# Kernel optimization log

Measured on AMD Instinct MI355X. Metric: run time of the kernel, lower is better.

## Reference

```python
import jax, jax.numpy as jnp
import numpy as np

N = 10000   # num_nodes (= input feature dim, identity-style features)
E = 320000  # edges (avg degree 32)
P = 200000  # candidate node pairs
H1, H2 = 32, 16


def gcn_conv(x, W, b, edge_index, num_nodes):
    # PyG GCNConv: add self-loops, symmetric D^-1/2 (A+I) D^-1/2 normalization,
    # linear transform, scatter-add aggregation, then bias.
    loop = jnp.arange(num_nodes)
    src = jnp.concatenate([edge_index[0], loop])
    dst = jnp.concatenate([edge_index[1], loop])
    deg = jax.ops.segment_sum(jnp.ones_like(src, dtype=x.dtype), dst,
                              num_segments=num_nodes)  # includes self-loop, so deg >= 1
    dinv = jax.lax.rsqrt(deg)
    norm = dinv[src] * dinv[dst]                       # [E+N]
    h = x @ W                                          # [N, out]
    out = jax.ops.segment_sum(h[src] * norm[:, None], dst, num_segments=num_nodes)
    return out + b


def setup_inputs() -> dict:
    key = jax.random.key(0)
    ks = jax.random.split(key, 9)
    x = jax.random.normal(ks[0], (N, N), dtype=jnp.float32)
    edge_index = jax.random.randint(ks[1], (2, E), 0, N)
    pair_index = jax.random.randint(ks[2], (P, 2), 0, N)
    W1 = jax.random.normal(ks[3], (N, H1), dtype=jnp.float32) * 0.01
    b1 = jnp.zeros((H1,), jnp.float32)
    W2 = jax.random.normal(ks[4], (H1, H2), dtype=jnp.float32) * 0.1
    b2 = jnp.zeros((H2,), jnp.float32)
    Wfc = jax.random.normal(ks[5], (2 * H2, 1), dtype=jnp.float32) * 0.1
    bfc = jnp.zeros((1,), jnp.float32)
    return {"x": x, "edge_index": edge_index, "pair_index": pair_index,
            "W1": W1, "b1": b1, "W2": W2, "b2": b2, "Wfc": Wfc, "bfc": bfc}


def reference(x, edge_index, pair_index, W1, b1, W2, b2, Wfc, bfc):
    h = jax.nn.relu(gcn_conv(x, W1, b1, edge_index, N))   # [N, 32]
    h = gcn_conv(h, W2, b2, edge_index, N)                # [N, 16]
    pair = jnp.concatenate([h[pair_index[:, 0]], h[pair_index[:, 1]]], axis=1)  # [P, 32]
    return jax.nn.sigmoid(pair @ Wfc + bfc)               # [P, 1]
```

## Files before the change

kernel.cpp:

```cpp
#include <hip/hip_runtime.h>
#include <math.h>

#define NN 10000
#define EE 320000
#define PP 200000

typedef __attribute__((ext_vector_type(8))) short bf8v;
typedef __attribute__((ext_vector_type(4))) float f4v;

#define GLOAD_LDS16(gsrc, ldst)                                                        \
    __builtin_amdgcn_global_load_lds((const __attribute__((address_space(1))) void*)(gsrc), \
                                     (__attribute__((address_space(3))) void*)(ldst), 16, 0, 0)

__device__ __forceinline__ ushort f2bf(float f) {
    uint u = __float_as_uint(f);
    return (ushort)((u + 0x7fffu + ((u >> 16) & 1u)) >> 16);
}

__global__ void k_deg_count(const int* __restrict__ dst, int* __restrict__ degi) {
    int e = blockIdx.x * blockDim.x + threadIdx.x;
    if (e < EE) atomicAdd(&degi[dst[e]], 1);
}

__global__ void k_dinv(const int* __restrict__ degi, float* __restrict__ dinv) {
    int n = blockIdx.x * blockDim.x + threadIdx.x;
    if (n < NN) dinv[n] = rsqrtf((float)(degi[n] + 1));
}

__global__ __launch_bounds__(256) void k_gemm1(const float* __restrict__ x,
                                               const float* __restrict__ W1,
                                               const float* __restrict__ zp,
                                               float* __restrict__ h1_pre) {
    __shared__ __align__(16) float  xs[2][128][32];
    __shared__ __align__(16) ushort wt[2][32][32];
    const int tid = threadIdx.x;
    const int lane = tid & 63;
    const int w = tid >> 6;
    const int lr = lane >> 3;
    const int s = lane & 7;
    const int row0 = blockIdx.x * 128;
    const int k_begin = blockIdx.y * 640;
    const int k_end = min(NN, k_begin + 640);
    const int ntiles = (k_end - k_begin + 31) >> 5;
    const long NN2 = (long)NN * NN;

    const int wc = tid & 31;
    const int wkq = tid >> 5;
    const int wt_off = wc * 32 + ((((wkq >> 1) ^ (wc & 3))) << 3) + ((wkq & 1) << 2);

    const int fl = lane & 15;
    const int khi = lane >> 4;

    f4v acc[2][2];
#pragma unroll
    for (int a = 0; a < 2; ++a)
#pragma unroll
        for (int b = 0; b < 2; ++b) acc[a][b] = (f4v){0.f, 0.f, 0.f, 0.f};

    auto stage_x = [&](int buf, int k0) {
#pragma unroll
        for (int j = 0; j < 4; ++j) {
            int r_local = w * 32 + j * 8 + lr;
            int c4 = s ^ (r_local & 7);
            long flat = (long)(row0 + r_local) * NN + k0 + c4 * 4;
            const float* src = (flat + 4 <= NN2) ? (x + flat) : zp;
            GLOAD_LDS16(src, &xs[buf][w * 32 + j * 8][0]);
        }
    };
    auto wload = [&](int k0, float* wr) {
#pragma unroll
        for (int i = 0; i < 4; ++i) {
            int gk = k0 + wkq * 4 + i;
            wr[i] = (gk < k_end) ? W1[(long)gk * 32 + wc] : 0.f;
        }
    };
    auto wstore = [&](int buf, const float* wr) {
        union { uint2 d; ushort u[4]; } p;
        p.u[0] = f2bf(wr[0]); p.u[1] = f2bf(wr[1]);
        p.u[2] = f2bf(wr[2]); p.u[3] = f2bf(wr[3]);
        *(uint2*)((ushort*)&wt[buf][0][0] + wt_off) = p.d;
    };
    auto compute = [&](int buf) {
        bf8v bfr[2];
        const int nb = fl & 3;
#pragma unroll
        for (int ct = 0; ct < 2; ++ct)
            bfr[ct] = *(const bf8v*)&wt[buf][ct * 16 + fl][(khi ^ nb) << 3];
#pragma unroll
        for (int rt = 0; rt < 2; ++rt) {
            const int row = w * 32 + rt * 16 + fl;
            const float4* xr = (const float4*)&xs[buf][row][0];
            float4 f0 = xr[(khi * 2) ^ (row & 7)];
            float4 f1 = xr[(khi * 2 + 1) ^ (row & 7)];
            union { bf8v v; ushort u[8]; } a;
            a.u[0] = f2bf(f0.x); a.u[1] = f2bf(f0.y); a.u[2] = f2bf(f0.z); a.u[3] = f2bf(f0.w);
            a.u[4] = f2bf(f1.x); a.u[5] = f2bf(f1.y); a.u[6] = f2bf(f1.z); a.u[7] = f2bf(f1.w);
#pragma unroll
            for (int ct = 0; ct < 2; ++ct)
                acc[rt][ct] = __builtin_amdgcn_mfma_f32_16x16x32_bf16(a.v, bfr[ct], acc[rt][ct], 0, 0, 0);
        }
    };

    float wr0[4], wr1[4];
    wload(k_begin, wr0);
    stage_x(0, k_begin);
    wstore(0, wr0);
    __syncthreads();

    int buf = 0;
    for (int t = 0; t < ntiles; ++t) {
        const int k0n = k_begin + (t + 1) * 32;
        if (t + 1 < ntiles) { wload(k0n, wr1); stage_x(buf ^ 1, k0n); }
        compute(buf);
        if (t + 1 < ntiles) wstore(buf ^ 1, wr1);
        __syncthreads();
        buf ^= 1;
    }

#pragma unroll
    for (int rt = 0; rt < 2; ++rt) {
        const int gbase = row0 + w * 32 + rt * 16 + khi * 4;
#pragma unroll
        for (int ct = 0; ct < 2; ++ct) {
            const int col = ct * 16 + fl;
#pragma unroll
            for (int r = 0; r < 4; ++r) {
                const int g = gbase + r;
                if (g < NN) atomicAdd(&h1_pre[g * 32 + col], acc[rt][ct][r]);
            }
        }
    }
}

__global__ void k_selfinit1(const float* __restrict__ h1_pre, const float* __restrict__ dinv,
                            float* __restrict__ out1) {
    int t = blockIdx.x * blockDim.x + threadIdx.x;
    if (t < NN * 32) {
        int n = t >> 5;
        float di = dinv[n];
        out1[t] = di * di * h1_pre[t];
    }
}

__global__ void k_scatter1(const int* __restrict__ src, const int* __restrict__ dst,
                           const float* __restrict__ dinv, const float* __restrict__ h1_pre,
                           float* __restrict__ out1) {
    int t = blockIdx.x * blockDim.x + threadIdx.x;
    if (t >= EE * 32) return;
    int e = t >> 5, c = t & 31;
    int s = src[e], d = dst[e];
    float nrm = dinv[s] * dinv[d];
    atomicAdd(&out1[d * 32 + c], h1_pre[s * 32 + c] * nrm);
}

__global__ void k_bias_relu1(float* __restrict__ out1, const float* __restrict__ b1) {
    int t = blockIdx.x * blockDim.x + threadIdx.x;
    if (t < NN * 32) out1[t] = fmaxf(out1[t] + b1[t & 31], 0.f);
}

__global__ __launch_bounds__(256) void k_gemm2(const float* __restrict__ out1,
                                               const float* __restrict__ W2,
                                               float* __restrict__ h2_pre) {
    __shared__ float w2s[512];
    int tid = threadIdx.x;
    w2s[tid] = W2[tid & 511];
    if (tid < 256) w2s[256 + tid] = W2[256 + tid];
    __syncthreads();
    int c = tid & 15, yloc = tid >> 4;
    int n = blockIdx.x * 16 + yloc;
    if (n < NN) {
        float a = 0.f;
#pragma unroll
        for (int k = 0; k < 32; ++k) a += out1[n * 32 + k] * w2s[k * 16 + c];
        h2_pre[n * 16 + c] = a;
    }
}

__global__ void k_selfinit2(const float* __restrict__ h2_pre, const float* __restrict__ dinv,
                            float* __restrict__ out2) {
    int t = blockIdx.x * blockDim.x + threadIdx.x;
    if (t < NN * 16) {
        int n = t >> 4;
        float di = dinv[n];
        out2[t] = di * di * h2_pre[t];
    }
}

__global__ void k_scatter2(const int* __restrict__ src, const int* __restrict__ dst,
                           const float* __restrict__ dinv, const float* __restrict__ h2_pre,
                           float* __restrict__ out2) {
    int t = blockIdx.x * blockDim.x + threadIdx.x;
    if (t >= EE * 16) return;
    int e = t >> 4, c = t & 15;
    int s = src[e], d = dst[e];
    float nrm = dinv[s] * dinv[d];
    atomicAdd(&out2[d * 16 + c], h2_pre[s * 16 + c] * nrm);
}

__global__ void k_final2(const float* __restrict__ out2, const float* __restrict__ b2,
                         const float* __restrict__ Wfc, float* __restrict__ s_arr,
                         float* __restrict__ t_arr) {
    int n = blockIdx.x * blockDim.x + threadIdx.x;
    if (n >= NN) return;
    float s = 0.f, t = 0.f;
#pragma unroll
    for (int c = 0; c < 16; ++c) {
        float v = out2[n * 16 + c] + b2[c];
        s += v * Wfc[c];
        t += v * Wfc[16 + c];
    }
    s_arr[n] = s;
    t_arr[n] = t;
}

__global__ void k_pairs(const int* __restrict__ pair, const float* __restrict__ s_arr,
                        const float* __restrict__ t_arr, const float* __restrict__ bfc,
                        float* __restrict__ out) {
    int p = blockIdx.x * blockDim.x + threadIdx.x;
    if (p >= PP) return;
    const int2 ab = ((const int2*)pair)[p];
    float z = s_arr[ab.x] + t_arr[ab.y] + bfc[0];
    out[p] = 1.f / (1.f + expf(-z));
}

extern "C" void kernel_launch(void* const* d_in, const int* in_sizes, int n_in,
                              void* d_out, int out_size, void* d_ws, size_t ws_size,
                              hipStream_t stream) {
    const float* x    = (const float*)d_in[0];
    const int*   edge = (const int*)d_in[1];
    const int*   pair = (const int*)d_in[2];
    const float* W1   = (const float*)d_in[3];
    const float* b1   = (const float*)d_in[4];
    const float* W2   = (const float*)d_in[5];
    const float* b2   = (const float*)d_in[6];
    const float* Wfc  = (const float*)d_in[7];
    const float* bfc  = (const float*)d_in[8];
    float* out = (float*)d_out;
    float* ws  = (float*)d_ws;

    const int* src = edge;
    const int* dst = edge + EE;

    int*   degi   = (int*)ws;
    float* dinv   = ws + NN;
    float* h1_pre = ws + 2 * NN;
    float* out1   = ws + 34 * NN;
    float* h2_pre = ws + 66 * NN;
    float* out2   = ws + 82 * NN;
    float* s_arr  = ws + 98 * NN;
    float* t_arr  = ws + 99 * NN;
    float* zp     = ws + 100 * NN;

    hipMemsetAsync(degi, 0, NN * sizeof(int), stream);
    hipMemsetAsync(h1_pre, 0, NN * 32 * sizeof(float), stream);
    hipMemsetAsync(zp, 0, 1024, stream);

    k_deg_count<<<(EE + 255) / 256, 256, 0, stream>>>(dst, degi);
    k_dinv<<<(NN + 255) / 256, 256, 0, stream>>>(degi, dinv);

    k_gemm1<<<dim3(79, 16), 256, 0, stream>>>(x, W1, zp, h1_pre);

    k_selfinit1<<<(NN * 32 + 255) / 256, 256, 0, stream>>>(h1_pre, dinv, out1);
    k_scatter1<<<(EE * 32 + 255) / 256, 256, 0, stream>>>(src, dst, dinv, h1_pre, out1);
    k_bias_relu1<<<(NN * 32 + 255) / 256, 256, 0, stream>>>(out1, b1);

    k_gemm2<<<(NN + 15) / 16, 256, 0, stream>>>(out1, W2, h2_pre);

    k_selfinit2<<<(NN * 16 + 255) / 256, 256, 0, stream>>>(h2_pre, dinv, out2);
    k_scatter2<<<(EE * 16 + 255) / 256, 256, 0, stream>>>(src, dst, dinv, h2_pre, out2);

    k_final2<<<(NN + 255) / 256, 256, 0, stream>>>(out2, b2, Wfc, s_arr, t_arr);
    k_pairs<<<(PP + 255) / 256, 256, 0, stream>>>(pair, s_arr, t_arr, bfc, out);
}
```

Baseline: 204.4 us.

## Pre-transpose W1 to bf16 and triple-buffer per-wave x staging without block syncs

Adds a prep kernel that transposes W1 to column-major bf16, so the GEMM loads B fragments straight from global memory into registers instead of converting and staging them through LDS. The x tiles are now staged per wave in a three-deep ring buffer, with a vmcnt wait replacing __syncthreads, which lets each wave prefetch two tiles ahead on its own. The aim is to remove block-wide barriers and the LDS round trip for weights, so the first GEMM streams the large x matrix closer to memory bandwidth. It costs an extra kernel launch, and the hand-written waitcnt depends on counting exactly how many loads are in flight.

```diff
diff --git a/kernel.cpp b/kernel.cpp
--- a/kernel.cpp
+++ b/kernel.cpp
@@ -4,6 +4,7 @@
 #define NN 10000
 #define EE 320000
 #define PP 200000
+#define WKP 10240
 
 typedef __attribute__((ext_vector_type(8))) short bf8v;
 typedef __attribute__((ext_vector_type(4))) float f4v;
@@ -27,99 +28,88 @@
     if (n < NN) dinv[n] = rsqrtf((float)(degi[n] + 1));
 }
 
+__global__ void k_wprep(const float* __restrict__ W1, ushort* __restrict__ w1t) {
+    int t = blockIdx.x * blockDim.x + threadIdx.x;
+    if (t >= 32 * WKP) return;
+    int c = t / WKP, k = t - c * WKP;
+    float v = (k < NN) ? W1[(long)k * 32 + c] : 0.f;
+    w1t[t] = f2bf(v);
+}
+
 __global__ __launch_bounds__(256) void k_gemm1(const float* __restrict__ x,
-                                               const float* __restrict__ W1,
+                                               const ushort* __restrict__ w1t,
                                                const float* __restrict__ zp,
                                                float* __restrict__ h1_pre) {
-    __shared__ __align__(16) float  xs[2][128][32];
-    __shared__ __align__(16) ushort wt[2][32][32];
+    __shared__ __align__(16) float xs[4][3][32][32];
     const int tid = threadIdx.x;
     const int lane = tid & 63;
     const int w = tid >> 6;
     const int lr = lane >> 3;
     const int s = lane & 7;
-    const int row0 = blockIdx.x * 128;
+    const int fl = lane & 15;
+    const int khi = lane >> 4;
+    const int row0 = blockIdx.x * 128 + w * 32;
     const int k_begin = blockIdx.y * 640;
     const int k_end = min(NN, k_begin + 640);
-    const int ntiles = (k_end - k_begin + 31) >> 5;
+    const int nt = (k_end - k_begin + 31) >> 5;
     const long NN2 = (long)NN * NN;
 
-    const int wc = tid & 31;
-    const int wkq = tid >> 5;
-    const int wt_off = wc * 32 + ((((wkq >> 1) ^ (wc & 3))) << 3) + ((wkq & 1) << 2);
-
-    const int fl = lane & 15;
-    const int khi = lane >> 4;
-
     f4v acc[2][2];
 #pragma unroll
     for (int a = 0; a < 2; ++a)
 #pragma unroll
         for (int b = 0; b < 2; ++b) acc[a][b] = (f4v){0.f, 0.f, 0.f, 0.f};
 
-    auto stage_x = [&](int buf, int k0) {
+    auto stage_x = [&](int buf, int t) {
+        const int k0 = k_begin + t * 32;
 #pragma unroll
         for (int j = 0; j < 4; ++j) {
-            int r_local = w * 32 + j * 8 + lr;
-            int c4 = s ^ (r_local & 7);
-            long flat = (long)(row0 + r_local) * NN + k0 + c4 * 4;
+            int rl = j * 8 + lr;
+            int c4 = s ^ (rl & 7);
+            long flat = (long)(row0 + rl) * NN + k0 + c4 * 4;
             const float* src = (flat + 4 <= NN2) ? (x + flat) : zp;
-            GLOAD_LDS16(src, &xs[buf][w * 32 + j * 8][0]);
+            GLOAD_LDS16(src, &xs[w][buf][j * 8][0]);
         }
     };
-    auto wload = [&](int k0, float* wr) {
-#pragma unroll
-        for (int i = 0; i < 4; ++i) {
-            int gk = k0 + wkq * 4 + i;
-            wr[i] = (gk < k_end) ? W1[(long)gk * 32 + wc] : 0.f;
-        }
+    auto wload = [&](int t, bf8v& b0, bf8v& b1) {
+        const long kg = (long)k_begin + t * 32 + khi * 8;
+        b0 = *(const bf8v*)(w1t + (long)(fl)      * WKP + kg);
+        b1 = *(const bf8v*)(w1t + (long)(16 + fl) * WKP + kg);
     };
-    auto wstore = [&](int buf, const float* wr) {
-        union { uint2 d; ushort u[4]; } p;
-        p.u[0] = f2bf(wr[0]); p.u[1] = f2bf(wr[1]);
-        p.u[2] = f2bf(wr[2]); p.u[3] = f2bf(wr[3]);
-        *(uint2*)((ushort*)&wt[buf][0][0] + wt_off) = p.d;
-    };
-    auto compute = [&](int buf) {
-        bf8v bfr[2];
-        const int nb = fl & 3;
-#pragma unroll
-        for (int ct = 0; ct < 2; ++ct)
-            bfr[ct] = *(const bf8v*)&wt[buf][ct * 16 + fl][(khi ^ nb) << 3];
+    auto compute = [&](int buf, bf8v b0, bf8v b1) {
 #pragma unroll
         for (int rt = 0; rt < 2; ++rt) {
-            const int row = w * 32 + rt * 16 + fl;
-            const float4* xr = (const float4*)&xs[buf][row][0];
-            float4 f0 = xr[(khi * 2) ^ (row & 7)];
-            float4 f1 = xr[(khi * 2 + 1) ^ (row & 7)];
+            const int rowl = rt * 16 + fl;
+            const float4* xr = (const float4*)&xs[w][buf][rowl][0];
+            float4 f0 = xr[(khi * 2)     ^ (rowl & 7)];
+            float4 f1 = xr[(khi * 2 + 1) ^ (rowl & 7)];
             union { bf8v v; ushort u[8]; } a;
             a.u[0] = f2bf(f0.x); a.u[1] = f2bf(f0.y); a.u[2] = f2bf(f0.z); a.u[3] = f2bf(f0.w);
             a.u[4] = f2bf(f1.x); a.u[5] = f2bf(f1.y); a.u[6] = f2bf(f1.z); a.u[7] = f2bf(f1.w);
-#pragma unroll
-            for (int ct = 0; ct < 2; ++ct)
-                acc[rt][ct] = __builtin_amdgcn_mfma_f32_16x16x32_bf16(a.v, bfr[ct], acc[rt][ct], 0, 0, 0);
+            acc[rt][0] = __builtin_amdgcn_mfma_f32_16x16x32_bf16(a.v, b0, acc[rt][0], 0, 0, 0);
+            acc[rt][1] = __builtin_amdgcn_mfma_f32_16x16x32_bf16(a.v, b1, acc[rt][1], 0, 0, 0);
         }
     };
 
-    float wr0[4], wr1[4];
-    wload(k_begin, wr0);
-    stage_x(0, k_begin);
-    wstore(0, wr0);
-    __syncthreads();
+    bf8v wc0, wc1, wn0, wn1;
+    stage_x(0, 0);
+    stage_x(1, 1);
+    wload(0, wc0, wc1);
 
     int buf = 0;
-    for (int t = 0; t < ntiles; ++t) {
-        const int k0n = k_begin + (t + 1) * 32;
-        if (t + 1 < ntiles) { wload(k0n, wr1); stage_x(buf ^ 1, k0n); }
-        compute(buf);
-        if (t + 1 < ntiles) wstore(buf ^ 1, wr1);
-        __syncthreads();
-        buf ^= 1;
+    for (int t = 0; t < nt; ++t) {
+        if (t + 2 < nt) stage_x((buf + 2 == 3 ? buf - 1 : buf + 2), t + 2);
+        if (t + 1 < nt) wload(t + 1, wn0, wn1);
+        asm volatile("s_waitcnt vmcnt(6)" ::: "memory");
+        __builtin_amdgcn_sched_barrier(0);
+        compute(buf, wc0, wc1);
+        wc0 = wn0; wc1 = wn1;
+        buf = (buf + 1 == 3) ? 0 : buf + 1;
     }
 
 #pragma unroll
     for (int rt = 0; rt < 2; ++rt) {
-        const int gbase = row0 + w * 32 + rt * 16 + khi * 4;
+        const int gbase = row0 + rt * 16 + khi * 4;
 #pragma unroll
         for (int ct = 0; ct < 2; ++ct) {
             const int col = ct * 16 + fl;
@@ -241,15 +231,16 @@
     const int* src = edge;
     const int* dst = edge + EE;
 
-    int*   degi   = (int*)ws;
-    float* dinv   = ws + NN;
-    float* h1_pre = ws + 2 * NN;
-    float* out1   = ws + 34 * NN;
-    float* h2_pre = ws + 66 * NN;
-    float* out2   = ws + 82 * NN;
-    float* s_arr  = ws + 98 * NN;
-    float* t_arr  = ws + 99 * NN;
-    float* zp     = ws + 100 * NN;
+    int*    degi   = (int*)ws;
+    float*  dinv   = ws + NN;
+    float*  h1_pre = ws + 2 * NN;
+    float*  out1   = ws + 34 * NN;
+    float*  h2_pre = ws + 66 * NN;
+    float*  out2   = ws + 82 * NN;
+    float*  s_arr  = ws + 98 * NN;
+    float*  t_arr  = ws + 99 * NN;
+    float*  zp     = ws + 100 * NN;
+    ushort* w1t    = (ushort*)(ws + 100 * NN + 256);
 
     hipMemsetAsync(degi, 0, NN * sizeof(int), stream);
     hipMemsetAsync(h1_pre, 0, NN * 32 * sizeof(float), stream);
@@ -257,8 +248,9 @@
 
     k_deg_count<<<(EE + 255) / 256, 256, 0, stream>>>(dst, degi);
     k_dinv<<<(NN + 255) / 256, 256, 0, stream>>>(degi, dinv);
-
-    k_gemm1<<<dim3(79, 16), 256, 0, stream>>>(x, W1, zp, h1_pre);
+    k_wprep<<<(32 * WKP + 255) / 256, 256, 0, stream>>>(W1, w1t);
+
+    k_gemm1<<<dim3(79, 16), 256, 0, stream>>>(x, w1t, zp, h1_pre);
 
     k_selfinit1<<<(NN * 32 + 255) / 256, 256, 0, stream>>>(h1_pre, dinv, out1);
     k_scatter1<<<(EE * 32 + 255) / 256, 256, 0, stream>>>(src, dst, dinv, h1_pre, out1);
```

New measurement: 207.3 us. Within noise of the previous version (+1.4%).
